# Kernel optimization log

Hardware: AMD Instinct MI355X
Metric: run time of the kernel (lower is better)

The kernel has to match this reference:

```python
import jax, jax.numpy as jnp
import numpy as np

N_NODES = 50000
N_EDGES = 800000
D_FEAT = 32
J = 4
NUM_GRAPHS = 64
MAX_SCALE = 2 ** (J - 1)  # 8 diffusion steps


def _propagate(x, src, dst, w):
    # gather x_j, weight per-edge, scatter-add into target nodes
    msgs = x[src] * w[:, None]
    return jax.ops.segment_sum(msgs, dst, num_segments=N_NODES)


def _diffuse(x, src, dst, w):
    outs = []
    x_curr = x
    for step in range(1, MAX_SCALE + 1):
        x_curr = _propagate(x_curr, src, dst, w)
        if step & (step - 1) == 0:  # collect at powers of two: 1,2,4,8 -> J scales
            outs.append(x_curr)
    return outs


def setup_inputs() -> dict:
    key = jax.random.key(0)
    k1, k2, k3, k4 = jax.random.split(key, 4)
    X = jax.random.normal(k1, (N_NODES, D_FEAT), dtype=jnp.float32)
    edge_index = jax.random.randint(k2, (2, N_EDGES), 0, N_NODES, dtype=jnp.int64)
    edge_weight = jax.random.uniform(k3, (N_EDGES,), dtype=jnp.float32)
    batch = jnp.sort(jax.random.randint(k4, (N_NODES,), 0, NUM_GRAPHS, dtype=jnp.int64))
    return {"X": X, "edge_index": edge_index, "edge_weight": edge_weight, "batch": batch}


def reference(X, edge_index, edge_weight, batch):
    src, dst = edge_index[0], edge_index[1]
    diff_list = _diffuse(X, src, dst, edge_weight)
    # F0: deepest scale
    F0 = diff_list[-1]
    # F1: first-order wavelet coefficients |psi_j x|
    F1 = jnp.concatenate(
        [jnp.abs(diff_list[i - 1] - diff_list[i]) for i in range(1, len(diff_list))],
        axis=1,
    )
    # F2: second-order, diffuse concatenated scales once more
    U = jnp.concatenate(diff_list, axis=1)  # [N, J*d]
    U_diff = _diffuse(U, src, dst, edge_weight)
    res = []
    for j in range(J):
        cs, ce = j * D_FEAT, (j + 1) * D_FEAT
        for jp in range(j + 1, J):
            res.append(jnp.abs(U_diff[jp][:, cs:ce] - U_diff[jp - 1][:, cs:ce]))
    F2 = jnp.concatenate(res, axis=1)
    feats = jnp.concatenate([F0, F1, F2], axis=1)  # [N, d*(1 + (J-1) + J*(J-1)/2)] = [N, 320]
    # global_mean_pool over batch assignment
    sums = jax.ops.segment_sum(feats, batch, num_segments=NUM_GRAPHS)
    counts = jax.ops.segment_sum(jnp.ones((feats.shape[0],), feats.dtype), batch, num_segments=NUM_GRAPHS)
    return sums / jnp.maximum(counts, 1.0)[:, None]
```

## Files before the change

### kernel.cpp

```cpp
#include <hip/hip_runtime.h>

#define N_NODES 50000
#define N_EDGES 800000
#define D_FEAT 32
#define NUM_GRAPHS 64
#define FEATS 320
#define NBIN 128
#define BINSH 9
#define CE 4096
#define NCHUNK ((N_EDGES + CE - 1) / CE)
#define NPB ((N_NODES + 511) / 512)

__device__ __forceinline__ unsigned short f2bf(float f) {
    unsigned int u = __float_as_uint(f);
    u = (u + 0x7fffu + ((u >> 16) & 1u)) >> 16;
    return (unsigned short)u;
}
__device__ __forceinline__ float bf2f(unsigned short h) {
    return __uint_as_float((unsigned int)h << 16);
}
__device__ __forceinline__ float bflo(unsigned int u) { return __uint_as_float(u << 16); }
__device__ __forceinline__ float bfhi(unsigned int u) { return __uint_as_float(u & 0xffff0000u); }


__global__ void binA_kernel(const int* __restrict__ dst, int* __restrict__ counts, int n) {
    __shared__ int h[NBIN];
    int t = threadIdx.x;
    if (t < NBIN) h[t] = 0;
    __syncthreads();
    int s0 = blockIdx.x * CE, e0 = min(s0 + CE, n);
    for (int i = s0 + t; i < e0; i += blockDim.x)
        atomicAdd(&h[dst[i] >> BINSH], 1);
    __syncthreads();
    if (t < NBIN) counts[blockIdx.x * NBIN + t] = h[t];
}

__global__ void binB_kernel(int* __restrict__ counts, int* __restrict__ binBase) {
    __shared__ int s[NBIN];
    int b = threadIdx.x;
    int tot = 0;
    #pragma unroll 8
    for (int c = 0; c < NCHUNK; ++c) tot += counts[c * NBIN + b];
    s[b] = tot;
    __syncthreads();
    for (int off = 1; off < NBIN; off <<= 1) {
        int u = (b >= off) ? s[b - off] : 0;
        __syncthreads();
        s[b] += u;
        __syncthreads();
    }
    int base = s[b] - tot;
    binBase[b] = base;
    if (b == NBIN - 1) binBase[NBIN] = s[b];
    int running = base;
    #pragma unroll 4
    for (int c = 0; c < NCHUNK; ++c) {
        int idx = c * NBIN + b;
        int v = counts[idx];
        counts[idx] = running;
        running += v;
    }
}

__global__ __launch_bounds__(256) void binC_kernel(const int* __restrict__ src,
                                                   const int* __restrict__ dst,
                                                   const float* __restrict__ w,
                                                   const int* __restrict__ counts,
                                                   int2* __restrict__ tmp, int n) {
    __shared__ int h[NBIN], sc[NBIN], cur[NBIN], gbase[NBIN];
    __shared__ int2 srec[CE];
    __shared__ unsigned char sbin[CE];
    int t = threadIdx.x;
    if (t < NBIN) h[t] = 0;
    __syncthreads();
    int s0 = blockIdx.x * CE, e0 = min(s0 + CE, n);
    int cnt = e0 - s0;
    for (int i = s0 + t; i < e0; i += blockDim.x)
        atomicAdd(&h[dst[i] >> BINSH], 1);
    __syncthreads();
    if (t < NBIN) sc[t] = h[t];
    __syncthreads();
    for (int off = 1; off < NBIN; off <<= 1) {
        int u = (t < NBIN && t >= off) ? sc[t - off] : 0;
        __syncthreads();
        if (t < NBIN) sc[t] += u;
        __syncthreads();
    }
    if (t < NBIN) {
        cur[t] = 0;
        gbase[t] = counts[blockIdx.x * NBIN + t];
    }
    __syncthreads();
    for (int i = s0 + t; i < e0; i += blockDim.x) {
        int d = dst[i];
        int b = d >> BINSH;
        int pos = (sc[b] - h[b]) + atomicAdd(&cur[b], 1);
        srec[pos] = make_int2(src[i] | ((int)f2bf(w[i]) << 16), d & 511);
        sbin[pos] = (unsigned char)b;
    }
    __syncthreads();
    for (int j = t; j < cnt; j += blockDim.x) {
        int b = sbin[j];
        tmp[gbase[b] + (j - (sc[b] - h[b]))] = srec[j];
    }
}

__global__ __launch_bounds__(256) void place_kernel(const int* __restrict__ binBase,
                                                    const int2* __restrict__ tmp,
                                                    unsigned int* __restrict__ edges,
                                                    int* __restrict__ rowptr, int n) {
    __shared__ int h[512], sc[512], cur[512];
    int b = blockIdx.x;
    int t = threadIdx.x;
    int base = binBase[b], end = binBase[b + 1];
    for (int i = t; i < 512; i += 256) { h[i] = 0; cur[i] = 0; }
    __syncthreads();
    for (int e = base + t; e < end; e += 256)
        atomicAdd(&h[tmp[e].y], 1);
    __syncthreads();
    for (int i = t; i < 512; i += 256) sc[i] = h[i];
    __syncthreads();
    for (int off = 1; off < 512; off <<= 1) {
        int i0 = t, i1 = t + 256;
        int a0 = (i0 >= off) ? sc[i0 - off] : 0;
        int a1 = (i1 >= off) ? sc[i1 - off] : 0;
        __syncthreads();
        sc[i0] += a0;
        sc[i1] += a1;
        __syncthreads();
    }
    int node0 = b << BINSH;
    for (int i = t; i < 512; i += 256) {
        int node = node0 + i;
        if (node <= n) rowptr[node] = base + sc[i] - h[i];
    }
    if (b == 0 && t == 0) rowptr[0] = 0;
    __syncthreads();
    for (int e = base + t; e < end; e += 256) {
        int2 p = tmp[e];
        int loc = p.y;
        int pos = base + (sc[loc] - h[loc]) + atomicAdd(&cur[loc], 1);
        edges[pos] = (unsigned int)p.x;
    }
}


__global__ void prep_kernel(const float4* __restrict__ xin, ushort4* __restrict__ xout,
                            const int* __restrict__ batch, int* __restrict__ gstart, int n) {
    int i = blockIdx.x * blockDim.x + threadIdx.x;
    if (i < n * 8) {
        float4 v = xin[i];
        ushort4 o;
        o.x = f2bf(v.x); o.y = f2bf(v.y); o.z = f2bf(v.z); o.w = f2bf(v.w);
        xout[i] = o;
    }
    if (i < n) {
        int g = batch[i];
        int gp = (i == 0) ? -1 : batch[i - 1];
        for (int gg = gp + 1; gg <= g; ++gg) gstart[gg] = i;
        if (i == n - 1)
            for (int gg = g + 1; gg <= NUM_GRAPHS; ++gg) gstart[gg] = n;
    }
}


__global__ __launch_bounds__(256, 4) void spmm_kernel(const uint4* __restrict__ xin,
                                                      uint4* __restrict__ yout,
                                                      const int* __restrict__ rowptr,
                                                      const unsigned int* __restrict__ edges,
                                                      int n) {
    int lane = threadIdx.x & 3;
    int node = (blockIdx.x * blockDim.x + threadIdx.x) >> 2;
    if (node >= n) return;
    int e0 = rowptr[node], e1 = rowptr[node + 1];
    float a0 = 0.f, a1 = 0.f, a2 = 0.f, a3 = 0.f;
    float a4 = 0.f, a5 = 0.f, a6 = 0.f, a7 = 0.f;
    int e = e0;
    int e16 = e0 + ((e1 - e0) & ~15);
    for (; e < e16; e += 16) {
        unsigned int r[16];
        #pragma unroll
        for (int u = 0; u < 16; ++u) r[u] = edges[e + u];
        uint4 v[16];
        #pragma unroll
        for (int u = 0; u < 16; ++u)
            v[u] = xin[(size_t)(r[u] & 0xffffu) * 4 + lane];
        #pragma unroll
        for (int u = 0; u < 16; ++u) {
            float w = bfhi(r[u]);
            a0 += bflo(v[u].x) * w; a1 += bfhi(v[u].x) * w;
            a2 += bflo(v[u].y) * w; a3 += bfhi(v[u].y) * w;
            a4 += bflo(v[u].z) * w; a5 += bfhi(v[u].z) * w;
            a6 += bflo(v[u].w) * w; a7 += bfhi(v[u].w) * w;
        }
    }
    int e4 = e0 + ((e1 - e0) & ~3);
    for (; e < e4; e += 4) {
        unsigned int r[4];
        #pragma unroll
        for (int u = 0; u < 4; ++u) r[u] = edges[e + u];
        uint4 v[4];
        #pragma unroll
        for (int u = 0; u < 4; ++u)
            v[u] = xin[(size_t)(r[u] & 0xffffu) * 4 + lane];
        #pragma unroll
        for (int u = 0; u < 4; ++u) {
            float w = bfhi(r[u]);
            a0 += bflo(v[u].x) * w; a1 += bfhi(v[u].x) * w;
            a2 += bflo(v[u].y) * w; a3 += bfhi(v[u].y) * w;
            a4 += bflo(v[u].z) * w; a5 += bfhi(v[u].z) * w;
            a6 += bflo(v[u].w) * w; a7 += bfhi(v[u].w) * w;
        }
    }
    for (; e < e1; ++e) {
        unsigned int r = edges[e];
        uint4 v = xin[(size_t)(r & 0xffffu) * 4 + lane];
        float w = bfhi(r);
        a0 += bflo(v.x) * w; a1 += bfhi(v.x) * w;
        a2 += bflo(v.y) * w; a3 += bfhi(v.y) * w;
        a4 += bflo(v.z) * w; a5 += bfhi(v.z) * w;
        a6 += bflo(v.w) * w; a7 += bfhi(v.w) * w;
    }
    uint4 o;
    o.x = (unsigned int)f2bf(a0) | ((unsigned int)f2bf(a1) << 16);
    o.y = (unsigned int)f2bf(a2) | ((unsigned int)f2bf(a3) << 16);
    o.z = (unsigned int)f2bf(a4) | ((unsigned int)f2bf(a5) << 16);
    o.w = (unsigned int)f2bf(a6) | ((unsigned int)f2bf(a7) << 16);
    yout[(size_t)node * 4 + lane] = o;
}


struct PoolPtrs { const unsigned short* a[10]; };

__global__ __launch_bounds__(256) void pool_kernel(PoolPtrs P, const int* __restrict__ gstart,
                                                   float* __restrict__ out) {
    __shared__ float red[8][FEATS];
    int t = threadIdx.x;
    int f = t & 31;
    int sub = t >> 5;
    int g = blockIdx.x >> 4;
    int s = blockIdx.x & 15;
    int gs = gstart[g], ge = gstart[g + 1];
    int len = ge - gs;
    int i0 = gs + ((len * s) >> 4);
    int i1 = gs + ((len * (s + 1)) >> 4);
    float acc[10];
    #pragma unroll
    for (int k = 0; k < 10; ++k) acc[k] = 0.f;
    for (int i = i0 + sub; i < i1; i += 8) {
        float v[10];
        #pragma unroll
        for (int k = 0; k < 10; ++k) v[k] = bf2f(P.a[k][(size_t)i * 32 + f]);
        acc[0] += v[6];
        acc[1] += fabsf(v[0] - v[1]);
        acc[2] += fabsf(v[1] - v[3]);
        acc[3] += fabsf(v[3] - v[6]);
        acc[4] += fabsf(v[2] - v[1]);
        acc[5] += fabsf(v[4] - v[2]);
        acc[6] += fabsf(v[7] - v[4]);
        acc[7] += fabsf(v[5] - v[3]);
        acc[8] += fabsf(v[8] - v[5]);
        acc[9] += fabsf(v[9] - v[6]);
    }
    #pragma unroll
    for (int k = 0; k < 10; ++k) red[sub][k * 32 + f] = acc[k];
    __syncthreads();
    float invl = 1.0f / (float)max(len, 1);
    for (int o = t; o < FEATS; o += 256) {
        float ssum = 0.f;
        #pragma unroll
        for (int j = 0; j < 8; ++j) ssum += red[j][o];
        if (ssum != 0.f || true) atomicAdd(&out[g * FEATS + o], ssum * invl);
    }
}


extern "C" void kernel_launch(void* const* d_in, const int* in_sizes, int n_in,
                              void* d_out, int out_size, void* d_ws, size_t ws_size,
                              hipStream_t stream) {
    const float* X     = (const float*)d_in[0];
    const int*   ei    = (const int*)d_in[1];
    const float* ew    = (const float*)d_in[2];
    const int*   batch = (const int*)d_in[3];
    float* out = (float*)d_out;

    const int N = N_NODES, E = N_EDGES;
    const int* src = ei;
    const int* dst = ei + E;

    char* base = (char*)d_ws;
    size_t off = 0;
    auto alloc = [&](size_t bytes) -> void* {
        void* p = base + off;
        off += (bytes + 255) & ~(size_t)255;
        return p;
    };
    unsigned short* y[13];
    for (int k = 0; k <= 12; ++k) y[k] = (unsigned short*)alloc((size_t)N * 32 * 2);

    int*  rowptr  = (int*)alloc((size_t)(N + 4) * 4);
    int*  gstart  = (int*)alloc((NUM_GRAPHS + 1) * 4);
    int*  counts  = (int*)alloc((size_t)NCHUNK * NBIN * 4);
    int*  binBase = (int*)alloc((NBIN + 1) * 4);
    int2* tmp     = (int2*)alloc((size_t)E * 8);
    unsigned int* edges = (unsigned int*)alloc((size_t)E * 4);

    hipMemsetAsync(out, 0, (size_t)out_size * 4, stream);

    binA_kernel<<<NCHUNK, 256, 0, stream>>>(dst, counts, E);
    binB_kernel<<<1, NBIN, 0, stream>>>(counts, binBase);
    binC_kernel<<<NCHUNK, 256, 0, stream>>>(src, dst, ew, counts, tmp, E);
    place_kernel<<<NPB, 256, 0, stream>>>(binBase, tmp, edges, rowptr, N);

    prep_kernel<<<(N * 8 + 255) / 256, 256, 0, stream>>>((const float4*)X, (ushort4*)y[0],
                                                         batch, gstart, N);

    const int SPMM_GRID = (N * 4 + 255) / 256;
    for (int k = 1; k <= 12; ++k) {
        spmm_kernel<<<SPMM_GRID, 256, 0, stream>>>((const uint4*)y[k - 1], (uint4*)y[k],
                                                   rowptr, edges, N);
    }

    {
        PoolPtrs p;
        const int idx[10] = {1, 2, 3, 4, 5, 6, 8, 9, 10, 12};
        for (int k = 0; k < 10; ++k) p.a[k] = y[idx[k]];
        pool_kernel<<<NUM_GRAPHS * 16, 256, 0, stream>>>(p, gstart, out);
    }
}
```

Measured before the change: 267.9 us.

## Split each node's SpMM row across 8 lanes with 8-byte loads, add nontemporal hints

The SpMM kernel now assigns 8 threads per node, each reading a ushort4 (4 bf16 features), where before 4 threads each read a uint4 (8 features). This doubles thread-level parallelism, halves the per-thread accumulator and register count, and shrinks the block to 128 threads. Edge loads and output stores now use nontemporal hints. The trade-off is twice as many edge-index loads per node, since each of the 8 lanes re-reads the edge list, plus narrower gather transactions.

```diff
diff --git a/kernel.cpp b/kernel.cpp
--- a/kernel.cpp
+++ b/kernel.cpp
@@ -11,6 +11,8 @@
 #define NCHUNK ((N_EDGES + CE - 1) / CE)
 #define NPB ((N_NODES + 511) / 512)
 
+typedef unsigned short ushort4v __attribute__((ext_vector_type(4)));
+
 __device__ __forceinline__ unsigned short f2bf(float f) {
     unsigned int u = __float_as_uint(f);
     u = (u + 0x7fffu + ((u >> 16) & 1u)) >> 16;
@@ -164,69 +166,63 @@
 }
 
 
-__global__ __launch_bounds__(256, 4) void spmm_kernel(const uint4* __restrict__ xin,
-                                                      uint4* __restrict__ yout,
+__global__ __launch_bounds__(128, 4) void spmm_kernel(const ushort4* __restrict__ xin,
+                                                      ushort4* __restrict__ yout,
                                                       const int* __restrict__ rowptr,
                                                       const unsigned int* __restrict__ edges,
                                                       int n) {
-    int lane = threadIdx.x & 3;
-    int node = (blockIdx.x * blockDim.x + threadIdx.x) >> 2;
+    int lane = threadIdx.x & 7;
+    int node = (blockIdx.x * blockDim.x + threadIdx.x) >> 3;
     if (node >= n) return;
     int e0 = rowptr[node], e1 = rowptr[node + 1];
     float a0 = 0.f, a1 = 0.f, a2 = 0.f, a3 = 0.f;
-    float a4 = 0.f, a5 = 0.f, a6 = 0.f, a7 = 0.f;
     int e = e0;
     int e16 = e0 + ((e1 - e0) & ~15);
     for (; e < e16; e += 16) {
         unsigned int r[16];
         #pragma unroll
-        for (int u = 0; u < 16; ++u) r[u] = edges[e + u];
-        uint4 v[16];
+        for (int u = 0; u < 16; ++u) r[u] = __builtin_nontemporal_load(&edges[e + u]);
+        ushort4 v[16];
         #pragma unroll
         for (int u = 0; u < 16; ++u)
-            v[u] = xin[(size_t)(r[u] & 0xffffu) * 4 + lane];
+            v[u] = xin[(size_t)(r[u] & 0xffffu) * 8 + lane];
         #pragma unroll
         for (int u = 0; u < 16; ++u) {
             float w = bfhi(r[u]);
-            a0 += bflo(v[u].x) * w; a1 += bfhi(v[u].x) * w;
-            a2 += bflo(v[u].y) * w; a3 += bfhi(v[u].y) * w;
-            a4 += bflo(v[u].z) * w; a5 += bfhi(v[u].z) * w;
-            a6 += bflo(v[u].w) * w; a7 += bfhi(v[u].w) * w;
+            a0 += bf2f(v[u].x) * w;
+            a1 += bf2f(v[u].y) * w;
+            a2 += bf2f(v[u].z) * w;
+            a3 += bf2f(v[u].w) * w;
         }
     }
     int e4 = e0 + ((e1 - e0) & ~3);
     for (; e < e4; e += 4) {
         unsigned int r[4];
         #pragma unroll
-        for (int u = 0; u < 4; ++u) r[u] = edges[e + u];
-        uint4 v[4];
+        for (int u = 0; u < 4; ++u) r[u] = __builtin_nontemporal_load(&edges[e + u]);
+        ushort4 v[4];
         #pragma unroll
         for (int u = 0; u < 4; ++u)
-            v[u] = xin[(size_t)(r[u] & 0xffffu) * 4 + lane];
+            v[u] = xin[(size_t)(r[u] & 0xffffu) * 8 + lane];
         #pragma unroll
         for (int u = 0; u < 4; ++u) {
             float w = bfhi(r[u]);
-            a0 += bflo(v[u].x) * w; a1 += bfhi(v[u].x) * w;
-            a2 += bflo(v[u].y) * w; a3 += bfhi(v[u].y) * w;
-            a4 += bflo(v[u].z) * w; a5 += bfhi(v[u].z) * w;
-            a6 += bflo(v[u].w) * w; a7 += bfhi(v[u].w) * w;
+            a0 += bf2f(v[u].x) * w;
+            a1 += bf2f(v[u].y) * w;
+            a2 += bf2f(v[u].z) * w;
+            a3 += bf2f(v[u].w) * w;
         }
     }
     for (; e < e1; ++e) {
-        unsigned int r = edges[e];
-        uint4 v = xin[(size_t)(r & 0xffffu) * 4 + lane];
+        unsigned int r = __builtin_nontemporal_load(&edges[e]);
+        ushort4 v = xin[(size_t)(r & 0xffffu) * 8 + lane];
         float w = bfhi(r);
-        a0 += bflo(v.x) * w; a1 += bfhi(v.x) * w;
-        a2 += bflo(v.y) * w; a3 += bfhi(v.y) * w;
-        a4 += bflo(v.z) * w; a5 += bfhi(v.z) * w;
-        a6 += bflo(v.w) * w; a7 += bfhi(v.w) * w;
-    }
-    uint4 o;
-    o.x = (unsigned int)f2bf(a0) | ((unsigned int)f2bf(a1) << 16);
-    o.y = (unsigned int)f2bf(a2) | ((unsigned int)f2bf(a3) << 16);
-    o.z = (unsigned int)f2bf(a4) | ((unsigned int)f2bf(a5) << 16);
-    o.w = (unsigned int)f2bf(a6) | ((unsigned int)f2bf(a7) << 16);
-    yout[(size_t)node * 4 + lane] = o;
+        a0 += bf2f(v.x) * w; a1 += bf2f(v.y) * w;
+        a2 += bf2f(v.z) * w; a3 += bf2f(v.w) * w;
+    }
+    ushort4v o;
+    o.x = f2bf(a0); o.y = f2bf(a1); o.z = f2bf(a2); o.w = f2bf(a3);
+    __builtin_nontemporal_store(o, (ushort4v*)&yout[(size_t)node * 8 + lane]);
 }
 
 
@@ -270,7 +266,7 @@
         float ssum = 0.f;
         #pragma unroll
         for (int j = 0; j < 8; ++j) ssum += red[j][o];
-        if (ssum != 0.f || true) atomicAdd(&out[g * FEATS + o], ssum * invl);
+        atomicAdd(&out[g * FEATS + o], ssum * invl);
     }
 }
 
@@ -315,9 +311,9 @@
     prep_kernel<<<(N * 8 + 255) / 256, 256, 0, stream>>>((const float4*)X, (ushort4*)y[0],
                                                          batch, gstart, N);
 
-    const int SPMM_GRID = (N * 4 + 255) / 256;
+    const int SPMM_GRID = (N * 8 + 127) / 128;
     for (int k = 1; k <= 12; ++k) {
-        spmm_kernel<<<SPMM_GRID, 256, 0, stream>>>((const uint4*)y[k - 1], (uint4*)y[k],
+        spmm_kernel<<<SPMM_GRID, 128, 0, stream>>>((const ushort4*)y[k - 1], (ushort4*)y[k],
                                                    rowptr, edges, N);
     }
 
```

Result: slower. 307.9 us (+14.9%).
